# Kernel tuning notes

Hardware: AMD Instinct MI355X
Metric: run time of the kernel (lower is better)

The kernel has to match this reference:

```python
import jax, jax.numpy as jnp
import numpy as np
import math

B, T, E, H = 2, 2048, 1024, 16
HD = E // H


def layernorm(x, g, b, eps=1e-5):
    mu = jnp.mean(x, axis=-1, keepdims=True)
    var = jnp.var(x, axis=-1, keepdims=True)
    return (x - mu) * jax.lax.rsqrt(var + eps) * g + b


def new_gelu(x):
    c = math.sqrt(2.0 / math.pi)
    return 0.5 * x * (1.0 + jnp.tanh(c * (x + 0.044715 * x ** 3)))


def setup_inputs() -> dict:
    key = jax.random.key(0)
    ks = jax.random.split(key, 6)
    s = 0.02
    return {
        "x": jax.random.normal(ks[0], (B, T, E), jnp.float32),
        "ln1_g": jnp.ones((E,), jnp.float32),
        "ln1_b": jnp.zeros((E,), jnp.float32),
        "w_attn": jax.random.normal(ks[1], (E, 3 * E), jnp.float32) * s,
        "b_attn": jnp.zeros((3 * E,), jnp.float32),
        "w_proj": jax.random.normal(ks[2], (E, E), jnp.float32) * s,
        "b_proj": jnp.zeros((E,), jnp.float32),
        "ln2_g": jnp.ones((E,), jnp.float32),
        "ln2_b": jnp.zeros((E,), jnp.float32),
        "w_fc": jax.random.normal(ks[3], (E, 4 * E), jnp.float32) * s,
        "b_fc": jnp.zeros((4 * E,), jnp.float32),
        "w_fc2": jax.random.normal(ks[4], (4 * E, E), jnp.float32) * s,
        "b_fc2": jnp.zeros((E,), jnp.float32),
    }


def reference(x, ln1_g, ln1_b, w_attn, b_attn, w_proj, b_proj,
              ln2_g, ln2_b, w_fc, b_fc, w_fc2, b_fc2):
    # --- attention branch (pre-norm) ---
    h = layernorm(x, ln1_g, ln1_b)
    qkv = h @ w_attn + b_attn                      # [B,T,3E]
    q, k, v = jnp.split(qkv, 3, axis=-1)
    # [B,T,E] -> [B,H,T,HD]
    q = q.reshape(B, T, H, HD).transpose(0, 2, 1, 3)
    k = k.reshape(B, T, H, HD).transpose(0, 2, 1, 3)
    v = v.reshape(B, T, H, HD).transpose(0, 2, 1, 3)
    att = jnp.einsum('bhqd,bhkd->bhqk', q, k) * (1.0 / math.sqrt(HD))
    causal = jnp.tril(jnp.ones((T, T), bool))       # [T,T]
    att = jnp.where(causal, att, -jnp.inf)
    att = jax.nn.softmax(att, axis=-1)
    y = jnp.einsum('bhqk,bhkd->bhqd', att, v)       # [B,H,T,HD]
    y = y.transpose(0, 2, 1, 3).reshape(B, T, E)
    y = y @ w_proj + b_proj
    x = x + y
    # --- MLP branch (pre-norm) ---
    h = layernorm(x, ln2_g, ln2_b)
    h = new_gelu(h @ w_fc + b_fc)
    h = h @ w_fc2 + b_fc2
    return x + h
```

## Files before the change

kernel.cpp:

```cpp
#include <hip/hip_runtime.h>

typedef unsigned short u16;
typedef unsigned int   u32;
typedef short bf16x8 __attribute__((ext_vector_type(8)));
typedef float f32x4  __attribute__((ext_vector_type(4)));

__device__ __forceinline__ float bf_lo(u32 u){ return __uint_as_float(u << 16); }
__device__ __forceinline__ float bf_hi(u32 u){ return __uint_as_float(u & 0xffff0000u); }
__device__ __forceinline__ u16 bf16r(float f){
  u32 u = __float_as_uint(f);
  u += 0x7fffu + ((u >> 16) & 1u);
  return (u16)(u >> 16);
}
__device__ __forceinline__ u32 pack2(float a, float b){
  return (u32)bf16r(a) | ((u32)bf16r(b) << 16);
}
__device__ __forceinline__ float gelu_f(float x){
  float t = 0.7978845608028654f * (x + 0.044715f * x * x * x);
  t = fminf(fmaxf(t, -12.f), 12.f);
  float e = __expf(2.f * t);
  float th = (e - 1.f) / (e + 1.f);
  return 0.5f * x * (1.f + th);
}
__device__ __forceinline__ void glds16(const void* g, void* l) {
  __builtin_amdgcn_global_load_lds(
      (const __attribute__((address_space(1))) void*)g,
      (__attribute__((address_space(3))) void*)l, 16, 0, 0);
}

__global__ __launch_bounds__(256) void wt_k(const float* __restrict__ W,
                                            u16* __restrict__ Wt, int K, int N) {
  __shared__ float t[32][33];
  int k0 = blockIdx.x * 32, n0 = blockIdx.y * 32;
  int tx = threadIdx.x & 31, ty = threadIdx.x >> 5;
  #pragma unroll
  for (int i = 0; i < 32; i += 8)
    t[ty + i][tx] = W[(size_t)(k0 + ty + i) * N + n0 + tx];
  __syncthreads();
  #pragma unroll
  for (int i = 0; i < 32; i += 8)
    Wt[(size_t)(n0 + ty + i) * K + k0 + tx] = bf16r(t[tx][ty + i]);
}

__global__ __launch_bounds__(256) void vt_k(const u16* __restrict__ qkv,
                                            u16* __restrict__ Vt) {
  __shared__ u16 tl[32][33];
  int t0 = blockIdx.x * 32;
  int bh = blockIdx.y >> 1, d0 = (blockIdx.y & 1) * 32;
  int bb = bh >> 4, h = bh & 15;
  int tx = threadIdx.x & 31, ty = threadIdx.x >> 5;
  #pragma unroll
  for (int i = 0; i < 32; i += 8)
    tl[ty + i][tx] = qkv[(size_t)(bb*2048 + t0 + ty + i)*3072 + 2048 + h*64 + d0 + tx];
  __syncthreads();
  #pragma unroll
  for (int i = 0; i < 32; i += 8)
    Vt[((size_t)bh*64 + d0 + ty + i)*2048 + t0 + tx] = tl[tx][ty + i];
}

__global__ __launch_bounds__(256) void ln_k(const float* __restrict__ x,
                                            const float* __restrict__ g,
                                            const float* __restrict__ bta,
                                            u16* __restrict__ out) {
  int row = blockIdx.x, tid = threadIdx.x;
  const float4 xv = ((const float4*)(x + (size_t)row * 1024))[tid];
  float s = xv.x + xv.y + xv.z + xv.w;
  float q = xv.x*xv.x + xv.y*xv.y + xv.z*xv.z + xv.w*xv.w;
  #pragma unroll
  for (int off = 32; off > 0; off >>= 1) {
    s += __shfl_down(s, off);
    q += __shfl_down(q, off);
  }
  __shared__ float ss[4], sq[4];
  if ((tid & 63) == 0) { ss[tid >> 6] = s; sq[tid >> 6] = q; }
  __syncthreads();
  s = ss[0] + ss[1] + ss[2] + ss[3];
  q = sq[0] + sq[1] + sq[2] + sq[3];
  float mu = s * (1.f/1024.f);
  float rs = rsqrtf(q * (1.f/1024.f) - mu*mu + 1e-5f);
  const float4 gv = ((const float4*)g)[tid];
  const float4 bv = ((const float4*)bta)[tid];
  uint2 o;
  o.x = pack2((xv.x-mu)*rs*gv.x + bv.x, (xv.y-mu)*rs*gv.y + bv.y);
  o.y = pack2((xv.z-mu)*rs*gv.z + bv.z, (xv.w-mu)*rs*gv.w + bv.w);
  ((uint2*)(out + (size_t)row * 1024))[tid] = o;
}

template<int MODE, int MI>
__global__ __launch_bounds__(256, 2) void gemm_k(
    const u16* __restrict__ A, const u16* __restrict__ Bt,
    const float* __restrict__ bias, const float* __restrict__ resid,
    void* __restrict__ out, int M, int N, int K)
{
  constexpr int TM = MI * 32;
  __shared__ u16 Al[TM * 64];
  __shared__ u16 Bl[128 * 64];
  const int tid = threadIdx.x;
  const int m0 = blockIdx.x * TM, n0 = blockIdx.y * 128;
  const int wave = tid >> 6, lane = tid & 63;
  const int wm = (wave >> 1) * (MI * 16), wn = (wave & 1) * 64;
  const int l15 = lane & 15, quad = lane >> 4;
  const int sr = lane >> 3, cs = lane & 7;
  f32x4 acc[MI][4];
  const f32x4 zero = {0.f, 0.f, 0.f, 0.f};
  #pragma unroll
  for (int i = 0; i < MI; ++i)
    #pragma unroll
    for (int j = 0; j < 4; ++j)
      acc[i][j] = zero;
  for (int k0 = 0; k0 < K; k0 += 64) {
    __syncthreads();
    #pragma unroll
    for (int it = 0; it < MI; ++it) {
      int r = it*32 + wave*8 + sr;
      int c = cs ^ (r & 7);
      glds16(&A[(size_t)(m0 + r) * K + k0 + c*8], &Al[(it*32 + wave*8) * 64]);
    }
    #pragma unroll
    for (int it = 0; it < 4; ++it) {
      int r = it*32 + wave*8 + sr;
      int c = cs ^ (r & 7);
      glds16(&Bt[(size_t)(n0 + r) * K + k0 + c*8], &Bl[(it*32 + wave*8) * 64]);
    }
    __syncthreads();
    #pragma unroll
    for (int kk = 0; kk < 2; ++kk) {
      bf16x8 af[MI], bfr[4];
      #pragma unroll
      for (int i = 0; i < MI; ++i) {
        int R = wm + i*16 + l15;
        af[i] = *(const bf16x8*)&Al[R*64 + ((kk*4 + quad) ^ (R & 7)) * 8];
      }
      #pragma unroll
      for (int j = 0; j < 4; ++j) {
        int R = wn + j*16 + l15;
        bfr[j] = *(const bf16x8*)&Bl[R*64 + ((kk*4 + quad) ^ (R & 7)) * 8];
      }
      #pragma unroll
      for (int i = 0; i < MI; ++i)
        #pragma unroll
        for (int j = 0; j < 4; ++j)
          acc[i][j] = __builtin_amdgcn_mfma_f32_16x16x32_bf16(af[i], bfr[j], acc[i][j], 0, 0, 0);
    }
  }
  #pragma unroll
  for (int i = 0; i < MI; ++i) {
    #pragma unroll
    for (int j = 0; j < 4; ++j) {
      int col = n0 + wn + j*16 + l15;
      float bv = bias[col];
      #pragma unroll
      for (int r = 0; r < 4; ++r) {
        int row = m0 + wm + i*16 + quad*4 + r;
        size_t idx = (size_t)row * N + col;
        float v = acc[i][j][r] + bv;
        if constexpr (MODE == 0)      ((u16*)out)[idx] = bf16r(v);
        else if constexpr (MODE == 1) ((float*)out)[idx] = v + resid[idx];
        else if constexpr (MODE == 2) ((u16*)out)[idx] = bf16r(gelu_f(v));
        else                          ((float*)out)[idx] = v + resid[idx];
      }
    }
  }
}

__global__ __launch_bounds__(256, 4) void attn_k(const u16* __restrict__ qkv,
                                                 const u16* __restrict__ Vt,
                                                 u16* __restrict__ y) {
  __shared__ u16 Kl[64*72];
  __shared__ u16 Vtl[64*72];
  __shared__ float Pl[4*16*68];
  const int tid = threadIdx.x;
  const int bh = blockIdx.x & 31, bb = bh >> 4, h = bh & 15;
  const int g = blockIdx.x >> 5;
  const int b4 = g >> 3;
  const int qt = (b4 == 1) ? (23 - g) : (b4 == 3) ? (55 - g) : g;
  const int w = tid >> 6, lane = tid & 63;
  const int l15 = lane & 15, quad = lane >> 4;
  float* Plw = Pl + w * (16*68);

  const u16* qp = qkv + ((size_t)(bb*2048 + qt*64 + w*16 + l15))*3072 + h*64 + quad*8;
  const bf16x8 aq0 = *(const bf16x8*)qp;
  const bf16x8 aq1 = *(const bf16x8*)(qp + 32);

  f32x4 o[4];
  const f32x4 zero = {0.f,0.f,0.f,0.f};
  #pragma unroll
  for (int dt = 0; dt < 4; ++dt) o[dt] = zero;
  float mrow[4] = {-1e30f,-1e30f,-1e30f,-1e30f};
  float lrow[4] = {0.f,0.f,0.f,0.f};

  for (int kt = 0; kt <= qt; ++kt) {
    __syncthreads();
    #pragma unroll
    for (int it = 0; it < 2; ++it) {
      int idx = it*256 + tid;
      int r = idx >> 3, c8 = idx & 7;
      *(uint4*)&Kl[r*72 + c8*8]  =
        *(const uint4*)&qkv[((size_t)(bb*2048 + kt*64 + r))*3072 + 1024 + h*64 + c8*8];
      *(uint4*)&Vtl[r*72 + c8*8] =
        *(const uint4*)&Vt[((size_t)bh*64 + r)*2048 + kt*64 + c8*8];
    }
    __syncthreads();
    f32x4 sv[4];
    #pragma unroll
    for (int nt = 0; nt < 4; ++nt) {
      f32x4 s = zero;
      const bf16x8 bk0 = *(const bf16x8*)&Kl[(nt*16 + l15)*72 + quad*8];
      const bf16x8 bk1 = *(const bf16x8*)&Kl[(nt*16 + l15)*72 + 32 + quad*8];
      s = __builtin_amdgcn_mfma_f32_16x16x32_bf16(aq0, bk0, s, 0, 0, 0);
      s = __builtin_amdgcn_mfma_f32_16x16x32_bf16(aq1, bk1, s, 0, 0, 0);
      int key = kt*64 + nt*16 + l15;
      #pragma unroll
      for (int r = 0; r < 4; ++r) {
        int qr = qt*64 + w*16 + quad*4 + r;
        sv[nt][r] = (key <= qr) ? s[r]*0.125f : -1e30f;
      }
    }
    float mc[4];
    #pragma unroll
    for (int r = 0; r < 4; ++r)
      mc[r] = fmaxf(fmaxf(sv[0][r],sv[1][r]), fmaxf(sv[2][r],sv[3][r]));
    #pragma unroll
    for (int off = 8; off >= 1; off >>= 1)
      #pragma unroll
      for (int r = 0; r < 4; ++r)
        mc[r] = fmaxf(mc[r], __shfl_xor(mc[r], off));
    float al[4];
    #pragma unroll
    for (int r = 0; r < 4; ++r) {
      float mn = fmaxf(mrow[r], mc[r]);
      al[r] = __expf(mrow[r] - mn);
      mrow[r] = mn;
      lrow[r] *= al[r];
    }
    #pragma unroll
    for (int dt = 0; dt < 4; ++dt)
      #pragma unroll
      for (int r = 0; r < 4; ++r)
        o[dt][r] *= al[r];
    #pragma unroll
    for (int nt = 0; nt < 4; ++nt)
      #pragma unroll
      for (int r = 0; r < 4; ++r)
        sv[nt][r] = __expf(sv[nt][r] - mrow[r]);
    float ls[4];
    #pragma unroll
    for (int r = 0; r < 4; ++r)
      ls[r] = (sv[0][r]+sv[1][r]) + (sv[2][r]+sv[3][r]);
    #pragma unroll
    for (int off = 8; off >= 1; off >>= 1)
      #pragma unroll
      for (int r = 0; r < 4; ++r)
        ls[r] += __shfl_xor(ls[r], off);
    #pragma unroll
    for (int r = 0; r < 4; ++r)
      lrow[r] += ls[r];
    #pragma unroll
    for (int nt = 0; nt < 4; ++nt)
      #pragma unroll
      for (int r = 0; r < 4; ++r)
        Plw[(quad*4+r)*68 + nt*16 + l15] = sv[nt][r];
    float4 pa = *(const float4*)&Plw[l15*68 + quad*8];
    float4 pb = *(const float4*)&Plw[l15*68 + quad*8 + 4];
    float4 pc = *(const float4*)&Plw[l15*68 + 32 + quad*8];
    float4 pd = *(const float4*)&Plw[l15*68 + 32 + quad*8 + 4];
    bf16x8 ap0, ap1;
    ((u32*)&ap0)[0] = pack2(pa.x, pa.y); ((u32*)&ap0)[1] = pack2(pa.z, pa.w);
    ((u32*)&ap0)[2] = pack2(pb.x, pb.y); ((u32*)&ap0)[3] = pack2(pb.z, pb.w);
    ((u32*)&ap1)[0] = pack2(pc.x, pc.y); ((u32*)&ap1)[1] = pack2(pc.z, pc.w);
    ((u32*)&ap1)[2] = pack2(pd.x, pd.y); ((u32*)&ap1)[3] = pack2(pd.z, pd.w);
    #pragma unroll
    for (int dt = 0; dt < 4; ++dt) {
      const bf16x8 bv0 = *(const bf16x8*)&Vtl[(dt*16 + l15)*72 + quad*8];
      const bf16x8 bv1 = *(const bf16x8*)&Vtl[(dt*16 + l15)*72 + 32 + quad*8];
      o[dt] = __builtin_amdgcn_mfma_f32_16x16x32_bf16(ap0, bv0, o[dt], 0, 0, 0);
      o[dt] = __builtin_amdgcn_mfma_f32_16x16x32_bf16(ap1, bv1, o[dt], 0, 0, 0);
    }
  }
  float inv[4];
  #pragma unroll
  for (int r = 0; r < 4; ++r) inv[r] = 1.f / lrow[r];
  #pragma unroll
  for (int dt = 0; dt < 4; ++dt)
    #pragma unroll
    for (int r = 0; r < 4; ++r) {
      int row = qt*64 + w*16 + quad*4 + r;
      y[((size_t)(bb*2048 + row))*1024 + h*64 + dt*16 + l15] = bf16r(o[dt][r] * inv[r]);
    }
}

extern "C" void kernel_launch(void* const* d_in, const int* in_sizes, int n_in,
                              void* d_out, int out_size, void* d_ws, size_t ws_size,
                              hipStream_t stream) {
  const float* x      = (const float*)d_in[0];
  const float* ln1_g  = (const float*)d_in[1];
  const float* ln1_b  = (const float*)d_in[2];
  const float* w_attn = (const float*)d_in[3];
  const float* b_attn = (const float*)d_in[4];
  const float* w_proj = (const float*)d_in[5];
  const float* b_proj = (const float*)d_in[6];
  const float* ln2_g  = (const float*)d_in[7];
  const float* ln2_b  = (const float*)d_in[8];
  const float* w_fc   = (const float*)d_in[9];
  const float* b_fc   = (const float*)d_in[10];
  const float* w_fc2  = (const float*)d_in[11];
  const float* b_fc2  = (const float*)d_in[12];

  char* ws = (char*)d_ws;
  u16*   wt_attn = (u16*)(ws);
  u16*   wt_proj = (u16*)(ws + 6291456);
  u16*   wt_fc   = (u16*)(ws + 8388608);
  u16*   wt_fc2  = (u16*)(ws + 16777216);
  u16*   h1      = (u16*)(ws + 25165824);
  u16*   qkvb    = (u16*)(ws + 33554432);
  u16*   yb      = (u16*)(ws + 58720256);
  float* x2      = (float*)(ws + 67108864);
  u16*   h2  = h1;
  u16*   vtb = h1;
  u16*   act = qkvb;

  wt_k<<<dim3(32, 96),  256, 0, stream>>>(w_attn, wt_attn, 1024, 3072);
  wt_k<<<dim3(32, 32),  256, 0, stream>>>(w_proj, wt_proj, 1024, 1024);
  wt_k<<<dim3(32, 128), 256, 0, stream>>>(w_fc,   wt_fc,   1024, 4096);
  wt_k<<<dim3(128, 32), 256, 0, stream>>>(w_fc2,  wt_fc2,  4096, 1024);

  ln_k<<<4096, 256, 0, stream>>>(x, ln1_g, ln1_b, h1);
  gemm_k<0,4><<<dim3(32, 24), 256, 0, stream>>>(h1, wt_attn, b_attn, nullptr,
                                                (void*)qkvb, 4096, 3072, 1024);
  vt_k<<<dim3(64, 64), 256, 0, stream>>>(qkvb, vtb);
  attn_k<<<dim3(1024), 256, 0, stream>>>(qkvb, vtb, yb);
  gemm_k<1,2><<<dim3(64, 8), 256, 0, stream>>>(yb, wt_proj, b_proj, x,
                                               (void*)x2, 4096, 1024, 1024);
  ln_k<<<4096, 256, 0, stream>>>(x2, ln2_g, ln2_b, h2);
  gemm_k<2,4><<<dim3(32, 32), 256, 0, stream>>>(h2, wt_fc, b_fc, nullptr,
                                                (void*)act, 4096, 4096, 1024);
  gemm_k<3,2><<<dim3(64, 8), 256, 0, stream>>>(act, wt_fc2, b_fc2, x2,
                                               d_out, 4096, 1024, 4096);
}
```

Before: 360.6 us.

## Restructure attention: 128-query tiles, async LDS loads, transposed MFMA, prescaled Q

Each attention block now processes two 64-row query groups against every K/V tile, so each loaded K/V tile is reused by twice as many queries. K/V tiles are loaded with global_load_lds into an XOR-swizzled layout. The QK product is computed transposed so that row reductions need only two cross-lane shuffles. The 1/sqrt(d)·log2(e) scale is folded into Q in the QKV GEMM epilogue, allowing exp2 to be used. P is stored as truncated bf16 rather than fp32, which halves LDS traffic for the P staging but adds a small accuracy risk. The causal mask is applied only on diagonal tiles. Occupancy drops because launch bounds fall to 2 blocks per SM and the grid is halved.

```diff
diff --git a/kernel.cpp b/kernel.cpp
--- a/kernel.cpp
+++ b/kernel.cpp
@@ -5,8 +5,6 @@
 typedef short bf16x8 __attribute__((ext_vector_type(8)));
 typedef float f32x4  __attribute__((ext_vector_type(4)));
 
-__device__ __forceinline__ float bf_lo(u32 u){ return __uint_as_float(u << 16); }
-__device__ __forceinline__ float bf_hi(u32 u){ return __uint_as_float(u & 0xffff0000u); }
 __device__ __forceinline__ u16 bf16r(float f){
   u32 u = __float_as_uint(f);
   u += 0x7fffu + ((u >> 16) & 1u);
@@ -14,6 +12,9 @@
 }
 __device__ __forceinline__ u32 pack2(float a, float b){
   return (u32)bf16r(a) | ((u32)bf16r(b) << 16);
+}
+__device__ __forceinline__ u32 pk_trunc(float a, float b){
+  return (__float_as_uint(a) >> 16) | (__float_as_uint(b) & 0xffff0000u);
 }
 __device__ __forceinline__ float gelu_f(float x){
   float t = 0.7978845608028654f * (x + 0.044715f * x * x * x);
@@ -27,6 +28,8 @@
       (const __attribute__((address_space(1))) void*)g,
       (__attribute__((address_space(3))) void*)l, 16, 0, 0);
 }
+
+#define QSCALE 0.1803368801111204f
 
 __global__ __launch_bounds__(256) void wt_k(const float* __restrict__ W,
                                             u16* __restrict__ Wt, int K, int N) {
@@ -149,6 +152,7 @@
     for (int j = 0; j < 4; ++j) {
       int col = n0 + wn + j*16 + l15;
       float bv = bias[col];
+      float sc = (MODE == 4 && col < 1024) ? QSCALE : 1.0f;
       #pragma unroll
       for (int r = 0; r < 4; ++r) {
         int row = m0 + wm + i*16 + quad*4 + r;
@@ -157,136 +161,143 @@
         if constexpr (MODE == 0)      ((u16*)out)[idx] = bf16r(v);
         else if constexpr (MODE == 1) ((float*)out)[idx] = v + resid[idx];
         else if constexpr (MODE == 2) ((u16*)out)[idx] = bf16r(gelu_f(v));
+        else if constexpr (MODE == 4) ((u16*)out)[idx] = bf16r(v * sc);
         else                          ((float*)out)[idx] = v + resid[idx];
       }
     }
   }
 }
 
-__global__ __launch_bounds__(256, 4) void attn_k(const u16* __restrict__ qkv,
+__global__ __launch_bounds__(256, 2) void attn_k(const u16* __restrict__ qkv,
                                                  const u16* __restrict__ Vt,
                                                  u16* __restrict__ y) {
-  __shared__ u16 Kl[64*72];
-  __shared__ u16 Vtl[64*72];
-  __shared__ float Pl[4*16*68];
+  __shared__ u16 Kl[64*64];
+  __shared__ u16 Vl[64*64];
+  __shared__ u16 Pw[4*16*72];
   const int tid = threadIdx.x;
   const int bh = blockIdx.x & 31, bb = bh >> 4, h = bh & 15;
-  const int g = blockIdx.x >> 5;
-  const int b4 = g >> 3;
-  const int qt = (b4 == 1) ? (23 - g) : (b4 == 3) ? (55 - g) : g;
+  const int tt = blockIdx.x >> 5;
+  const int qt = (tt < 8) ? tt : 23 - tt;
   const int w = tid >> 6, lane = tid & 63;
   const int l15 = lane & 15, quad = lane >> 4;
-  float* Plw = Pl + w * (16*68);
-
-  const u16* qp = qkv + ((size_t)(bb*2048 + qt*64 + w*16 + l15))*3072 + h*64 + quad*8;
-  const bf16x8 aq0 = *(const bf16x8*)qp;
-  const bf16x8 aq1 = *(const bf16x8*)(qp + 32);
-
-  f32x4 o[4];
+  const int sr = lane >> 3, cs = lane & 7;
+  u16* Pme = Pw + w * (16*72);
+
+  bf16x8 aq[2][2];
+  #pragma unroll
+  for (int g = 0; g < 2; ++g) {
+    const u16* qp = qkv + ((size_t)(bb*2048 + qt*128 + g*64 + w*16 + l15))*3072
+                    + h*64 + quad*8;
+    aq[g][0] = *(const bf16x8*)qp;
+    aq[g][1] = *(const bf16x8*)(qp + 32);
+  }
+  f32x4 o[2][4];
   const f32x4 zero = {0.f,0.f,0.f,0.f};
   #pragma unroll
-  for (int dt = 0; dt < 4; ++dt) o[dt] = zero;
-  float mrow[4] = {-1e30f,-1e30f,-1e30f,-1e30f};
-  float lrow[4] = {0.f,0.f,0.f,0.f};
-
-  for (int kt = 0; kt <= qt; ++kt) {
+  for (int g = 0; g < 2; ++g)
+    #pragma unroll
+    for (int dt = 0; dt < 4; ++dt) o[g][dt] = zero;
+  float m[2] = {-1e30f, -1e30f}, l[2] = {0.f, 0.f};
+  const int w16l = w*16 + l15;
+  const int dquad = quad*4;
+
+  for (int kt = 0; kt <= 2*qt + 1; ++kt) {
     __syncthreads();
     #pragma unroll
     for (int it = 0; it < 2; ++it) {
-      int idx = it*256 + tid;
-      int r = idx >> 3, c8 = idx & 7;
-      *(uint4*)&Kl[r*72 + c8*8]  =
-        *(const uint4*)&qkv[((size_t)(bb*2048 + kt*64 + r))*3072 + 1024 + h*64 + c8*8];
-      *(uint4*)&Vtl[r*72 + c8*8] =
-        *(const uint4*)&Vt[((size_t)bh*64 + r)*2048 + kt*64 + c8*8];
+      int r = it*32 + w*8 + sr;
+      int c = cs ^ (r & 7);
+      glds16(&qkv[((size_t)(bb*2048 + kt*64 + r))*3072 + 1024 + h*64 + c*8],
+             &Kl[(it*32 + w*8) * 64]);
+      glds16(&Vt[((size_t)(bh*64 + r))*2048 + kt*64 + c*8],
+             &Vl[(it*32 + w*8) * 64]);
     }
     __syncthreads();
-    f32x4 sv[4];
+    bf16x8 ak[4][2], av[4][2];
     #pragma unroll
     for (int nt = 0; nt < 4; ++nt) {
-      f32x4 s = zero;
-      const bf16x8 bk0 = *(const bf16x8*)&Kl[(nt*16 + l15)*72 + quad*8];
-      const bf16x8 bk1 = *(const bf16x8*)&Kl[(nt*16 + l15)*72 + 32 + quad*8];
-      s = __builtin_amdgcn_mfma_f32_16x16x32_bf16(aq0, bk0, s, 0, 0, 0);
-      s = __builtin_amdgcn_mfma_f32_16x16x32_bf16(aq1, bk1, s, 0, 0, 0);
-      int key = kt*64 + nt*16 + l15;
-      #pragma unroll
-      for (int r = 0; r < 4; ++r) {
-        int qr = qt*64 + w*16 + quad*4 + r;
-        sv[nt][r] = (key <= qr) ? s[r]*0.125f : -1e30f;
-      }
-    }
-    float mc[4];
-    #pragma unroll
-    for (int r = 0; r < 4; ++r)
-      mc[r] = fmaxf(fmaxf(sv[0][r],sv[1][r]), fmaxf(sv[2][r],sv[3][r]));
-    #pragma unroll
-    for (int off = 8; off >= 1; off >>= 1)
-      #pragma unroll
-      for (int r = 0; r < 4; ++r)
-        mc[r] = fmaxf(mc[r], __shfl_xor(mc[r], off));
-    float al[4];
-    #pragma unroll
-    for (int r = 0; r < 4; ++r) {
-      float mn = fmaxf(mrow[r], mc[r]);
-      al[r] = __expf(mrow[r] - mn);
-      mrow[r] = mn;
-      lrow[r] *= al[r];
-    }
-    #pragma unroll
-    for (int dt = 0; dt < 4; ++dt)
-      #pragma unroll
-      for (int r = 0; r < 4; ++r)
-        o[dt][r] *= al[r];
-    #pragma unroll
-    for (int nt = 0; nt < 4; ++nt)
-      #pragma unroll
-      for (int r = 0; r < 4; ++r)
-        sv[nt][r] = __expf(sv[nt][r] - mrow[r]);
-    float ls[4];
-    #pragma unroll
-    for (int r = 0; r < 4; ++r)
-      ls[r] = (sv[0][r]+sv[1][r]) + (sv[2][r]+sv[3][r]);
-    #pragma unroll
-    for (int off = 8; off >= 1; off >>= 1)
-      #pragma unroll
-      for (int r = 0; r < 4; ++r)
-        ls[r] += __shfl_xor(ls[r], off);
-    #pragma unroll
-    for (int r = 0; r < 4; ++r)
-      lrow[r] += ls[r];
-    #pragma unroll
-    for (int nt = 0; nt < 4; ++nt)
-      #pragma unroll
-      for (int r = 0; r < 4; ++r)
-        Plw[(quad*4+r)*68 + nt*16 + l15] = sv[nt][r];
-    float4 pa = *(const float4*)&Plw[l15*68 + quad*8];
-    float4 pb = *(const float4*)&Plw[l15*68 + quad*8 + 4];
-    float4 pc = *(const float4*)&Plw[l15*68 + 32 + quad*8];
-    float4 pd = *(const float4*)&Plw[l15*68 + 32 + quad*8 + 4];
-    bf16x8 ap0, ap1;
-    ((u32*)&ap0)[0] = pack2(pa.x, pa.y); ((u32*)&ap0)[1] = pack2(pa.z, pa.w);
-    ((u32*)&ap0)[2] = pack2(pb.x, pb.y); ((u32*)&ap0)[3] = pack2(pb.z, pb.w);
-    ((u32*)&ap1)[0] = pack2(pc.x, pc.y); ((u32*)&ap1)[1] = pack2(pc.z, pc.w);
-    ((u32*)&ap1)[2] = pack2(pd.x, pd.y); ((u32*)&ap1)[3] = pack2(pd.z, pd.w);
+      int R = nt*16 + l15;
+      #pragma unroll
+      for (int kk = 0; kk < 2; ++kk) {
+        ak[nt][kk] = *(const bf16x8*)&Kl[R*64 + ((kk*4 + quad) ^ (R & 7)) * 8];
+        av[nt][kk] = *(const bf16x8*)&Vl[R*64 + ((kk*4 + quad) ^ (R & 7)) * 8];
+      }
+    }
+    #pragma unroll
+    for (int g = 0; g < 2; ++g) {
+      if (kt > 2*qt + g) continue;
+      f32x4 sv[4];
+      #pragma unroll
+      for (int nt = 0; nt < 4; ++nt) {
+        f32x4 s = zero;
+        s = __builtin_amdgcn_mfma_f32_16x16x32_bf16(ak[nt][0], aq[g][0], s, 0, 0, 0);
+        s = __builtin_amdgcn_mfma_f32_16x16x32_bf16(ak[nt][1], aq[g][1], s, 0, 0, 0);
+        sv[nt] = s;
+      }
+      if (kt == 2*qt + g) {
+        #pragma unroll
+        for (int nt = 0; nt < 4; ++nt)
+          #pragma unroll
+          for (int r = 0; r < 4; ++r)
+            if (nt*16 + dquad + r > w16l) sv[nt][r] = -1e30f;
+      }
+      float mc = fmaxf(fmaxf(fmaxf(sv[0][0],sv[0][1]),fmaxf(sv[0][2],sv[0][3])),
+                       fmaxf(fmaxf(sv[1][0],sv[1][1]),fmaxf(sv[1][2],sv[1][3])));
+      float mc2= fmaxf(fmaxf(fmaxf(sv[2][0],sv[2][1]),fmaxf(sv[2][2],sv[2][3])),
+                       fmaxf(fmaxf(sv[3][0],sv[3][1]),fmaxf(sv[3][2],sv[3][3])));
+      mc = fmaxf(mc, mc2);
+      mc = fmaxf(mc, __shfl_xor(mc, 16));
+      mc = fmaxf(mc, __shfl_xor(mc, 32));
+      float mn = fmaxf(m[g], mc);
+      float alpha = exp2f(m[g] - mn);
+      m[g] = mn;
+      l[g] *= alpha;
+      #pragma unroll
+      for (int dt = 0; dt < 4; ++dt)
+        #pragma unroll
+        for (int r = 0; r < 4; ++r)
+          o[g][dt][r] *= alpha;
+      float p[4][4];
+      #pragma unroll
+      for (int nt = 0; nt < 4; ++nt)
+        #pragma unroll
+        for (int r = 0; r < 4; ++r)
+          p[nt][r] = exp2f(sv[nt][r] - mn);
+      float ps = ((p[0][0]+p[0][1])+(p[0][2]+p[0][3]))
+               + ((p[1][0]+p[1][1])+(p[1][2]+p[1][3]))
+               + ((p[2][0]+p[2][1])+(p[2][2]+p[2][3]))
+               + ((p[3][0]+p[3][1])+(p[3][2]+p[3][3]));
+      ps += __shfl_xor(ps, 16);
+      ps += __shfl_xor(ps, 32);
+      l[g] += ps;
+      #pragma unroll
+      for (int nt = 0; nt < 4; ++nt) {
+        uint2 pr;
+        pr.x = pk_trunc(p[nt][0], p[nt][1]);
+        pr.y = pk_trunc(p[nt][2], p[nt][3]);
+        *(uint2*)&Pme[l15*72 + nt*16 + dquad] = pr;
+      }
+      const bf16x8 bp0 = *(const bf16x8*)&Pme[l15*72 + quad*8];
+      const bf16x8 bp1 = *(const bf16x8*)&Pme[l15*72 + 32 + quad*8];
+      #pragma unroll
+      for (int dt = 0; dt < 4; ++dt) {
+        o[g][dt] = __builtin_amdgcn_mfma_f32_16x16x32_bf16(av[dt][0], bp0, o[g][dt], 0, 0, 0);
+        o[g][dt] = __builtin_amdgcn_mfma_f32_16x16x32_bf16(av[dt][1], bp1, o[g][dt], 0, 0, 0);
+      }
+    }
+  }
+  #pragma unroll
+  for (int g = 0; g < 2; ++g) {
+    float inv = 1.f / l[g];
+    u16* yp = y + ((size_t)(bb*2048 + qt*128 + g*64 + w*16 + l15))*1024 + h*64;
     #pragma unroll
     for (int dt = 0; dt < 4; ++dt) {
-      const bf16x8 bv0 = *(const bf16x8*)&Vtl[(dt*16 + l15)*72 + quad*8];
-      const bf16x8 bv1 = *(const bf16x8*)&Vtl[(dt*16 + l15)*72 + 32 + quad*8];
-      o[dt] = __builtin_amdgcn_mfma_f32_16x16x32_bf16(ap0, bv0, o[dt], 0, 0, 0);
-      o[dt] = __builtin_amdgcn_mfma_f32_16x16x32_bf16(ap1, bv1, o[dt], 0, 0, 0);
-    }
-  }
-  float inv[4];
-  #pragma unroll
-  for (int r = 0; r < 4; ++r) inv[r] = 1.f / lrow[r];
-  #pragma unroll
-  for (int dt = 0; dt < 4; ++dt)
-    #pragma unroll
-    for (int r = 0; r < 4; ++r) {
-      int row = qt*64 + w*16 + quad*4 + r;
-      y[((size_t)(bb*2048 + row))*1024 + h*64 + dt*16 + l15] = bf16r(o[dt][r] * inv[r]);
-    }
+      uint2 pk;
+      pk.x = pack2(o[g][dt][0]*inv, o[g][dt][1]*inv);
+      pk.y = pack2(o[g][dt][2]*inv, o[g][dt][3]*inv);
+      *(uint2*)(yp + dt*16 + dquad) = pk;
+    }
+  }
 }
 
 extern "C" void kernel_launch(void* const* d_in, const int* in_sizes, int n_in,
@@ -325,10 +336,10 @@
   wt_k<<<dim3(128, 32), 256, 0, stream>>>(w_fc2,  wt_fc2,  4096, 1024);
 
   ln_k<<<4096, 256, 0, stream>>>(x, ln1_g, ln1_b, h1);
-  gemm_k<0,4><<<dim3(32, 24), 256, 0, stream>>>(h1, wt_attn, b_attn, nullptr,
+  gemm_k<4,4><<<dim3(32, 24), 256, 0, stream>>>(h1, wt_attn, b_attn, nullptr,
                                                 (void*)qkvb, 4096, 3072, 1024);
   vt_k<<<dim3(64, 64), 256, 0, stream>>>(qkvb, vtb);
-  attn_k<<<dim3(1024), 256, 0, stream>>>(qkvb, vtb, yb);
+  attn_k<<<dim3(512), 256, 0, stream>>>(qkvb, vtb, yb);
   gemm_k<1,2><<<dim3(64, 8), 256, 0, stream>>>(yb, wt_proj, b_proj, x,
                                                (void*)x2, 4096, 1024, 1024);
   ln_k<<<4096, 256, 0, stream>>>(x2, ln2_g, ln2_b, h2);
```

Result: faster. 353.2 us (-2.0%).
